# Kernel tuning notes

Measured on AMD Instinct MI355X. Metric: run time of the kernel, lower is better.

The kernel has to match this reference:

```python
import jax, jax.numpy as jnp
import numpy as np

DIM = 1024
B, L = 8, 2048
ACT = DIM // 4          # sparse_ratio 0.25
HID = DIM // 4          # LowRankFF reduction 4
EPS = 1e-6
K, DILATION = 5, 1
PAD = (K - 1) * DILATION // 2


def setup_inputs() -> dict:
    key = jax.random.key(0)
    ks = jax.random.split(key, 16)
    s = lambda fan_in: 1.0 / np.sqrt(fan_in)
    return {
        "x": jax.random.normal(ks[0], (B, L, DIM), jnp.float32),
        "norm_w": jnp.ones((DIM,), jnp.float32),
        "dw_w": jax.random.normal(ks[1], (DIM, 1, K), jnp.float32) * s(K),
        "dw_b": jax.random.normal(ks[2], (DIM,), jnp.float32) * s(K),
        "pw_w": jax.random.normal(ks[3], (DIM, DIM), jnp.float32) * s(DIM),
        "pw_b": jax.random.normal(ks[4], (DIM,), jnp.float32) * s(DIM),
        "alpha": jnp.full((ACT,), 0.9, jnp.float32),
        "beta": jnp.full((ACT,), 0.1, jnp.float32),
        "W1_w": jax.random.normal(ks[5], (DIM, DIM), jnp.float32) * s(DIM),
        "W1_b": jax.random.normal(ks[6], (DIM,), jnp.float32) * s(DIM),
        "W2_w": jax.random.normal(ks[7], (DIM, DIM), jnp.float32) * s(DIM),
        "W2_b": jax.random.normal(ks[8], (DIM,), jnp.float32) * s(DIM),
        "down_w": jax.random.normal(ks[9], (HID, DIM), jnp.float32) * s(DIM),
        "down_b": jax.random.normal(ks[10], (HID,), jnp.float32) * s(DIM),
        "up_w": jax.random.normal(ks[11], (DIM, HID), jnp.float32) * s(HID),
        "up_b": jax.random.normal(ks[12], (DIM,), jnpp := jnp.float32) * s(HID),
    }


def reference(x, norm_w, dw_w, dw_b, pw_w, pw_b, alpha, beta,
              W1_w, W1_b, W2_w, W2_b, down_w, down_b, up_w, up_b):
    residual = x
    # RMSNorm
    rms = jnp.sqrt(jnp.mean(x * x, axis=-1, keepdims=True) + EPS)
    xn = norm_w * (x / rms)                              # [B,L,D]
    # depthwise conv (groups=DIM), NCH layout; same-length output
    xc = jax.lax.conv_general_dilated(
        xn.transpose(0, 2, 1), dw_w,
        window_strides=(1,), padding=[(PAD, PAD)],
        rhs_dilation=(DILATION,), feature_group_count=DIM,
        dimension_numbers=("NCH", "OIH", "NCH")) + dw_b[None, :, None]
    xc = xc.transpose(0, 2, 1)                           # [B,L,D]
    # pointwise conv == dense linear over channels
    x_conv = jnp.einsum("bld,od->blo", xc, pw_w) + pw_b
    # sparse shift-gate recurrence on FIRST ACT channels (faithful to source)
    x_act = xn[:, :, :ACT]                               # [B,L,A]

    def step(h, xt):                                     # h,xt: [B,A]
        h = alpha * h + beta * xt
        return h, h

    _, hs = jax.lax.scan(step, jnp.zeros((B, ACT), xn.dtype),
                         x_act.transpose(1, 0, 2))       # hs: [L,B,A]
    x_rec = jnp.concatenate([hs.transpose(1, 0, 2), xn[:, :, ACT:]], axis=-1)
    # gated fusion
    y = x_conv + x_rec
    y = y + jax.nn.sigmoid(y @ W1_w.T + W1_b) * jnp.tanh(y @ W2_w.T + W2_b)
    # low-rank FF (exact gelu, matching torch F.gelu default)
    y = y + (jax.nn.gelu(y @ down_w.T + down_b, approximate=False) @ up_w.T + up_b)
    return y + residual
```

## Files before the change

kernel.cpp:

```cpp
#include <hip/hip_runtime.h>
#include <math.h>

#define DIMC 1024
#define BB   8
#define LL   2048
#define ACTC 256
#define HIDC 256
#define EPSV 1e-6f
#define MROWS (BB * LL)
#define NCHUNK 32
#define LC     64

typedef __bf16 bf16x8 __attribute__((ext_vector_type(8)));
typedef float  f32x4  __attribute__((ext_vector_type(4)));

__device__ __forceinline__ unsigned short f2bf(float f) {
    union { float f; unsigned int u; } v; v.f = f;
    unsigned int u = v.u + 0x7fffu + ((v.u >> 16) & 1u);
    return (unsigned short)(u >> 16);
}
__device__ __forceinline__ float bf2f(unsigned short s) {
    union { float f; unsigned int u; } v; v.u = ((unsigned int)s) << 16;
    return v.f;
}
__device__ __forceinline__ float fast_sigmoid(float x) {
    return 1.0f / (1.0f + __expf(-x));
}
__device__ __forceinline__ float fast_tanh(float x) {
    float ax = fabsf(x);
    float t = 1.0f - 2.0f / (__expf(2.0f * ax) + 1.0f);
    return copysignf(t, x);
}

__global__ void k_convert5(const float* __restrict__ s0, const float* __restrict__ s1,
                           const float* __restrict__ s2, const float* __restrict__ s3,
                           const float* __restrict__ s4,
                           unsigned short* __restrict__ d0, unsigned short* __restrict__ d1,
                           unsigned short* __restrict__ d2, unsigned short* __restrict__ d3,
                           unsigned short* __restrict__ d4) {
    int i = blockIdx.x * blockDim.x + threadIdx.x;
    if (i < 1048576)            d0[i]           = f2bf(s0[i]);
    else if (i < 2097152)       d1[i - 1048576] = f2bf(s1[i - 1048576]);
    else if (i < 3145728)       d2[i - 2097152] = f2bf(s2[i - 2097152]);
    else if (i < 3407872)       d3[i - 3145728] = f2bf(s3[i - 3145728]);
    else if (i < 3670016)       d4[i - 3407872] = f2bf(s4[i - 3407872]);
}

__global__ __launch_bounds__(256) void k_rmsnorm(const float* __restrict__ x,
                                                 const float* __restrict__ w,
                                                 unsigned short* __restrict__ xnb) {
    int m = blockIdx.x;
    int t = threadIdx.x;
    float4 v = ((const float4*)(x + (size_t)m * DIMC))[t];
    float ss = v.x*v.x + v.y*v.y + v.z*v.z + v.w*v.w;
#pragma unroll
    for (int off = 32; off > 0; off >>= 1) ss += __shfl_down(ss, off, 64);
    __shared__ float sred[4];
    if ((t & 63) == 0) sred[t >> 6] = ss;
    __syncthreads();
    float tot = sred[0] + sred[1] + sred[2] + sred[3];
    float rinv = 1.0f / sqrtf(tot * (1.0f / DIMC) + EPSV);
    float4 wv = ((const float4*)w)[t];
    uint2 o;
    o.x = (unsigned)f2bf(wv.x * v.x * rinv) | ((unsigned)f2bf(wv.y * v.y * rinv) << 16);
    o.y = (unsigned)f2bf(wv.z * v.z * rinv) | ((unsigned)f2bf(wv.w * v.w * rinv) << 16);
    ((uint2*)(xnb + (size_t)m * DIMC))[t] = o;
}

__global__ __launch_bounds__(256) void k_dwconv(const unsigned short* __restrict__ xnb,
                                                const float* __restrict__ dww,
                                                const float* __restrict__ dwb,
                                                unsigned short* __restrict__ xc) {
    int m = blockIdx.x;
    int l = m & (LL - 1);
    int t = threadIdx.x;
    int c0 = t * 4;
    float wgt[4][5];
#pragma unroll
    for (int j = 0; j < 4; ++j)
#pragma unroll
        for (int k = 0; k < 5; ++k) wgt[j][k] = dww[(c0 + j) * 5 + k];
    float4 bv = ((const float4*)dwb)[t];
    float acc[4] = {bv.x, bv.y, bv.z, bv.w};
#pragma unroll
    for (int k = 0; k < 5; ++k) {
        int ll = l + k - 2;
        if (ll < 0 || ll >= LL) continue;
        uint2 rv = ((const uint2*)(xnb + (size_t)(m + k - 2) * DIMC))[t];
        acc[0] += bf2f((unsigned short)(rv.x & 0xffff)) * wgt[0][k];
        acc[1] += bf2f((unsigned short)(rv.x >> 16))    * wgt[1][k];
        acc[2] += bf2f((unsigned short)(rv.y & 0xffff)) * wgt[2][k];
        acc[3] += bf2f((unsigned short)(rv.y >> 16))    * wgt[3][k];
    }
    uint2 o;
    o.x = (unsigned)f2bf(acc[0]) | ((unsigned)f2bf(acc[1]) << 16);
    o.y = (unsigned)f2bf(acc[2]) | ((unsigned)f2bf(acc[3]) << 16);
    ((uint2*)(xc + (size_t)m * DIMC))[t] = o;
}

__global__ __launch_bounds__(256) void k_scan_a(const unsigned short* __restrict__ xnb,
                                                const float* __restrict__ alpha,
                                                const float* __restrict__ beta,
                                                float* __restrict__ F) {
    int blk = blockIdx.x;
    int b = blk >> 5, k = blk & (NCHUNK - 1);
    int c = threadIdx.x;
    float a = alpha[c], bt = beta[c];
    const unsigned short* p = xnb + ((size_t)(b * LL + k * LC)) * DIMC + c;
    float h = 0.0f;
    for (int l = 0; l < LC; ++l) h = a * h + bt * bf2f(p[(size_t)l * DIMC]);
    F[(size_t)blk * ACTC + c] = h;
}
__global__ __launch_bounds__(256) void k_scan_b(const float* __restrict__ alpha,
                                                const float* __restrict__ F,
                                                float* __restrict__ Cv) {
    int b = blockIdx.x;
    int c = threadIdx.x;
    float a = alpha[c];
    float aL = a;
#pragma unroll
    for (int i = 0; i < 6; ++i) aL *= aL;
    float T = 0.0f;
    for (int k = 0; k < NCHUNK; ++k) {
        size_t idx = ((size_t)b * NCHUNK + k) * ACTC + c;
        Cv[idx] = T;
        T = F[idx] + aL * T;
    }
}
__global__ __launch_bounds__(256) void k_scan_c(const unsigned short* __restrict__ xnb,
                                                const float* __restrict__ alpha,
                                                const float* __restrict__ beta,
                                                const float* __restrict__ Cv,
                                                unsigned short* __restrict__ hs) {
    int blk = blockIdx.x;
    int b = blk >> 5, k = blk & (NCHUNK - 1);
    int c = threadIdx.x;
    float a = alpha[c], bt = beta[c];
    const unsigned short* p = xnb + ((size_t)(b * LL + k * LC)) * DIMC + c;
    unsigned short*       q = hs  + ((size_t)(b * LL + k * LC)) * ACTC + c;
    float h = Cv[(size_t)blk * ACTC + c];
    for (int l = 0; l < LC; ++l) {
        h = a * h + bt * bf2f(p[(size_t)l * DIMC]);
        q[(size_t)l * ACTC] = f2bf(h);
    }
}

#define TM 128
#define TN 128
#define BK 64

#define GLOAD_LDS(gp, lp) \
    __builtin_amdgcn_global_load_lds((const __attribute__((address_space(1))) unsigned int*)(gp), \
                                     (__attribute__((address_space(3))) unsigned int*)(lp), 16, 0, 0)

template<int MODE>
__global__ __launch_bounds__(256, (MODE == 1) ? 2 : 4) void k_gemm(
        const unsigned short* __restrict__ A,
        const unsigned short* __restrict__ B0,
        const unsigned short* __restrict__ B1,
        const float* __restrict__ bias0,
        const float* __restrict__ bias1,
        const unsigned short* __restrict__ add0,
        const unsigned short* __restrict__ add1,
        const float* __restrict__ addf,
        float* __restrict__ outf,
        unsigned short* __restrict__ outb,
        int M, int N, int K)
{
    constexpr int LDSB = (MODE == 1) ? 49152 : 32768;
    __shared__ __align__(16) char lds[LDSB];
    unsigned short* sA  = (unsigned short*)lds;
    unsigned short* sB0 = (unsigned short*)(lds + 16384);
    unsigned short* sB1 = (unsigned short*)(lds + 32768);

    int nx = gridDim.x;
    int bid = blockIdx.y * nx + blockIdx.x;
    int xcd = bid & 7, s = bid >> 3;
    int colt = s % nx, rowgrp = s / nx;
    int m0 = (rowgrp * 8 + xcd) * TM;
    int n0 = colt * TN;

    int t = threadIdx.x;
    int w = t >> 6, lane = t & 63;
    int wm = (w >> 1) * 64, wn = (w & 1) * 64;
    int quad = lane >> 4, lm = lane & 15;
    int lm7 = lm & 7;

    f32x4 zero = {0.f, 0.f, 0.f, 0.f};
    f32x4 acc0[4][4];
    f32x4 acc1[(MODE == 1) ? 4 : 1][(MODE == 1) ? 4 : 1];
#pragma unroll
    for (int i = 0; i < 4; ++i)
#pragma unroll
        for (int j = 0; j < 4; ++j) acc0[i][j] = zero;
    if constexpr (MODE == 1) {
#pragma unroll
        for (int i = 0; i < 4; ++i)
#pragma unroll
            for (int j = 0; j < 4; ++j) acc1[i][j] = zero;
    }

    for (int k0 = 0; k0 < K; k0 += BK) {
        __syncthreads();
#pragma unroll
        for (int c = 0; c < 4; ++c) {
            int i = t + c * 256;
            int r = i >> 3;
            int sc = ((i & 7) ^ (r & 7)) << 3;
            GLOAD_LDS(A  + (size_t)(m0 + r) * K + k0 + sc, sA  + i * 8);
            GLOAD_LDS(B0 + (size_t)(n0 + r) * K + k0 + sc, sB0 + i * 8);
            if constexpr (MODE == 1)
                GLOAD_LDS(B1 + (size_t)(n0 + r) * K + k0 + sc, sB1 + i * 8);
        }
        __syncthreads();

#pragma unroll
        for (int ks = 0; ks < BK; ks += 32) {
            int cgb = ks >> 3;
            bf16x8 af[4], b0f[4];
#pragma unroll
            for (int i = 0; i < 4; ++i) {
                int sg = ((cgb + quad) ^ lm7) << 3;
                af[i]  = *(const bf16x8*)(sA  + (wm + i * 16 + lm) * BK + sg);
                b0f[i] = *(const bf16x8*)(sB0 + (wn + i * 16 + lm) * BK + sg);
            }
            if constexpr (MODE == 1) {
                bf16x8 b1f[4];
#pragma unroll
                for (int i = 0; i < 4; ++i)
                    b1f[i] = *(const bf16x8*)(sB1 + (wn + i * 16 + lm) * BK + (((cgb + quad) ^ lm7) << 3));
#pragma unroll
                for (int mi = 0; mi < 4; ++mi)
#pragma unroll
                    for (int ni = 0; ni < 4; ++ni) {
                        acc0[mi][ni] = __builtin_amdgcn_mfma_f32_16x16x32_bf16(af[mi], b0f[ni], acc0[mi][ni], 0, 0, 0);
                        acc1[mi][ni] = __builtin_amdgcn_mfma_f32_16x16x32_bf16(af[mi], b1f[ni], acc1[mi][ni], 0, 0, 0);
                    }
            } else {
#pragma unroll
                for (int mi = 0; mi < 4; ++mi)
#pragma unroll
                    for (int ni = 0; ni < 4; ++ni)
                        acc0[mi][ni] = __builtin_amdgcn_mfma_f32_16x16x32_bf16(af[mi], b0f[ni], acc0[mi][ni], 0, 0, 0);
            }
        }
    }

    __syncthreads();
    if constexpr (MODE == 3) {
        float* sO = (float*)lds;
#pragma unroll
        for (int half = 0; half < 2; ++half) {
            if (wm == half * 64) {
#pragma unroll
                for (int mi = 0; mi < 4; ++mi) {
#pragma unroll
                    for (int ni = 0; ni < 4; ++ni) {
                        int nl = wn + ni * 16 + lm;
                        float bn = bias0[n0 + nl];
#pragma unroll
                        for (int j = 0; j < 4; ++j) {
                            int mloc = mi * 16 + quad * 4 + j;
                            sO[mloc * TN + nl] = acc0[mi][ni][j] + bn;
                        }
                    }
                }
            }
            __syncthreads();
#pragma unroll
            for (int c = 0; c < 8; ++c) {
                int i = t + c * 256;
                int r = i >> 5, c4 = (i & 31) << 2;
                int m = m0 + half * 64 + r, n = n0 + c4;
                float4 v  = *(float4*)(sO + r * TN + c4);
                uint2  ab = *(const uint2*)(add0 + (size_t)m * N + n);
                float4 xf = *(const float4*)(addf + (size_t)m * N + n);
                float4 o;
                o.x = v.x + bf2f((unsigned short)(ab.x & 0xffff)) + xf.x;
                o.y = v.y + bf2f((unsigned short)(ab.x >> 16))    + xf.y;
                o.z = v.z + bf2f((unsigned short)(ab.y & 0xffff)) + xf.z;
                o.w = v.w + bf2f((unsigned short)(ab.y >> 16))    + xf.w;
                *(float4*)(outf + (size_t)m * N + n) = o;
            }
            __syncthreads();
        }
    } else {
        unsigned short* sO = (unsigned short*)lds;
#pragma unroll
        for (int mi = 0; mi < 4; ++mi) {
#pragma unroll
            for (int ni = 0; ni < 4; ++ni) {
                int nl = wn + ni * 16 + lm;
                int n  = n0 + nl;
                float bn = bias0[n];
                float bn1 = (MODE == 1) ? bias1[n] : 0.0f;
#pragma unroll
                for (int j = 0; j < 4; ++j) {
                    int ml = wm + mi * 16 + quad * 4 + j;
                    float v = acc0[mi][ni][j];
                    float r;
                    if constexpr (MODE == 0) {
                        r = v + bn;
                    } else if constexpr (MODE == 1) {
                        float u1 = v + bn;
                        float u2 = acc1[mi][ni][j] + bn1;
                        r = fast_sigmoid(u1) * fast_tanh(u2);
                    } else {
                        float u = v + bn;
                        r = 0.5f * u * (1.0f + erff(u * 0.70710678118654752f));
                    }
                    sO[ml * TN + nl] = f2bf(r);
                }
            }
        }
        __syncthreads();
#pragma unroll
        for (int c = 0; c < 8; ++c) {
            int i = t + c * 256;
            int r = i >> 4, c8 = (i & 15) << 3;
            int m = m0 + r, n = n0 + c8;
            uint4 g = *(uint4*)(sO + r * TN + c8);
            if constexpr (MODE == 2) {
                *(uint4*)(outb + (size_t)m * N + n) = g;
            } else {
                uint4 av;
                if constexpr (MODE == 0) {
                    av = (n0 < ACTC) ? *(const uint4*)(add0 + (size_t)m * ACTC + n)
                                     : *(const uint4*)(add1 + (size_t)m * DIMC + n);
                } else {
                    av = *(const uint4*)(add0 + (size_t)m * N + n);
                }
                unsigned* gp = (unsigned*)&g;
                unsigned* ap = (unsigned*)&av;
                uint4 o;
                unsigned* op = (unsigned*)&o;
#pragma unroll
                for (int q = 0; q < 4; ++q) {
                    float lo = bf2f((unsigned short)(gp[q] & 0xffff)) + bf2f((unsigned short)(ap[q] & 0xffff));
                    float hi = bf2f((unsigned short)(gp[q] >> 16))    + bf2f((unsigned short)(ap[q] >> 16));
                    op[q] = (unsigned)f2bf(lo) | ((unsigned)f2bf(hi) << 16);
                }
                *(uint4*)(outb + (size_t)m * N + n) = o;
            }
        }
    }
}

extern "C" void kernel_launch(void* const* d_in, const int* in_sizes, int n_in,
                              void* d_out, int out_size, void* d_ws, size_t ws_size,
                              hipStream_t stream) {
    (void)in_sizes; (void)n_in; (void)out_size; (void)ws_size;
    const float* x      = (const float*)d_in[0];
    const float* norm_w = (const float*)d_in[1];
    const float* dw_w   = (const float*)d_in[2];
    const float* dw_b   = (const float*)d_in[3];
    const float* pw_w   = (const float*)d_in[4];
    const float* pw_b   = (const float*)d_in[5];
    const float* alpha  = (const float*)d_in[6];
    const float* beta   = (const float*)d_in[7];
    const float* W1_w   = (const float*)d_in[8];
    const float* W1_b   = (const float*)d_in[9];
    const float* W2_w   = (const float*)d_in[10];
    const float* W2_b   = (const float*)d_in[11];
    const float* down_w = (const float*)d_in[12];
    const float* down_b = (const float*)d_in[13];
    const float* up_w   = (const float*)d_in[14];
    const float* up_b   = (const float*)d_in[15];

    char* ws = (char*)d_ws;
    unsigned short* xnb  = (unsigned short*)(ws);
    unsigned short* xc   = (unsigned short*)(ws + 33554432ull);
    unsigned short* hs   = (unsigned short*)(ws + 67108864ull);
    unsigned short* y1b  = (unsigned short*)(ws + 75497472ull);
    unsigned short* y2b  = (unsigned short*)(ws + 109051904ull);
    unsigned short* gact = (unsigned short*)(ws + 142606336ull);
    unsigned short* wpw  = (unsigned short*)(ws + 150994944ull);
    unsigned short* w1b  = wpw + 1048576;
    unsigned short* w2b  = w1b + 1048576;
    unsigned short* wdn  = w2b + 1048576;
    unsigned short* wup  = wdn + 262144;
    float*          Fb   = (float*)(ws + 159383552ull);
    float*          Cb   = (float*)(ws + 159383552ull + 262144ull);

    k_convert5<<<14336, 256, 0, stream>>>(pw_w, W1_w, W2_w, down_w, up_w,
                                          wpw, w1b, w2b, wdn, wup);

    k_rmsnorm<<<MROWS, 256, 0, stream>>>(x, norm_w, xnb);
    k_dwconv <<<MROWS, 256, 0, stream>>>(xnb, dw_w, dw_b, xc);

    k_scan_a<<<BB * NCHUNK, ACTC, 0, stream>>>(xnb, alpha, beta, Fb);
    k_scan_b<<<BB, ACTC, 0, stream>>>(alpha, Fb, Cb);
    k_scan_c<<<BB * NCHUNK, ACTC, 0, stream>>>(xnb, alpha, beta, Cb, hs);

    dim3 g1(DIMC / TN, MROWS / TM);
    dim3 g2(HIDC / TN, MROWS / TM);
    k_gemm<0><<<g1, 256, 0, stream>>>(xc, wpw, nullptr, pw_b, nullptr, hs, xnb, nullptr, nullptr, y1b, MROWS, DIMC, DIMC);
    k_gemm<1><<<g1, 256, 0, stream>>>(y1b, w1b, w2b, W1_b, W2_b, y1b, nullptr, nullptr, nullptr, y2b, MROWS, DIMC, DIMC);
    k_gemm<2><<<g2, 256, 0, stream>>>(y2b, wdn, nullptr, down_b, nullptr, nullptr, nullptr, nullptr, nullptr, gact, MROWS, HIDC, DIMC);
    k_gemm<3><<<g1, 256, 0, stream>>>(gact, wup, nullptr, up_b, nullptr, y2b, nullptr, x, (float*)d_out, nullptr, MROWS, DIMC, HIDC);
}
```

Baseline: 375.5 us.

## Replace pointwise and gated GEMMs with 256-row tiled direct-to-LDS pipelined kernel

```diff
diff --git a/kernel.cpp b/kernel.cpp
--- a/kernel.cpp
+++ b/kernel.cpp
@@ -343,6 +343,206 @@
                 *(uint4*)(outb + (size_t)m * N + n) = o;
             }
         }
+    }
+}
+
+
+#define STG8(gb, rb, kq, dsto) \
+    __builtin_amdgcn_global_load_lds( \
+        (const __attribute__((address_space(1))) unsigned int*)((gb) + (size_t)(rb) * DIMC + (kq)), \
+        (__attribute__((address_space(3))) unsigned int*)(sb + (dsto) + (rb) * 64 + t * 8), 16, 0, 0)
+
+#define FENCE asm volatile("" ::: "memory")
+#define BAR   do { FENCE; __builtin_amdgcn_s_barrier(); FENCE; } while (0)
+
+#define READ_A(h, s) \
+    do { \
+        _Pragma("unroll") \
+        for (int i = 0; i < 4; ++i) { \
+            int ar = wm * 128 + (h) * 64 + i * 16 + lm; \
+            af[i] = *(const bf16x8*)(sb + bO + ar * 64 + ((((s) * 4 + quad) ^ lm7) << 3)); \
+        } \
+    } while (0)
+
+#define PHASE_MFMA(h, s) \
+    do { \
+        __builtin_amdgcn_s_setprio(1); \
+        _Pragma("unroll") \
+        for (int i = 0; i < 4; ++i) { \
+            _Pragma("unroll") \
+            for (int j = 0; j < NBF; ++j) { \
+                acc0[(h) * 4 + i][j] = __builtin_amdgcn_mfma_f32_16x16x32_bf16(af[i], bf0[s][j], acc0[(h) * 4 + i][j], 0, 0, 0); \
+                if constexpr (MODE == 1) \
+                    acc1[(h) * 4 + i][j] = __builtin_amdgcn_mfma_f32_16x16x32_bf16(af[i], bf1[s][j], acc1[(h) * 4 + i][j], 0, 0, 0); \
+            } \
+        } \
+        __builtin_amdgcn_s_setprio(0); \
+    } while (0)
+
+template<int MODE>
+__global__ __launch_bounds__(512, 1) void k_gemm8(
+        const unsigned short* __restrict__ A,
+        const unsigned short* __restrict__ B0,
+        const unsigned short* __restrict__ B1,
+        const float* __restrict__ bias0,
+        const float* __restrict__ bias1,
+        const unsigned short* __restrict__ add0,
+        const unsigned short* __restrict__ add1,
+        unsigned short* __restrict__ outb)
+{
+    constexpr int BN  = (MODE == 1) ? 128 : 256;
+    constexpr int WBN = BN / 4;
+    constexpr int NBF = WBN / 16;
+    constexpr int NTN = DIMC / BN;
+    constexpr int NT  = DIMC / 64;
+
+    extern __shared__ __align__(16) char lds[];
+    unsigned short* sb = (unsigned short*)lds;
+
+    int bid = blockIdx.x;
+    int xcd = bid & 7, sgrp = bid >> 3;
+    int colt = sgrp % NTN, rowgrp = sgrp / NTN;
+    int m0 = (rowgrp * 8 + xcd) * 256;
+    int n0 = colt * BN;
+
+    int t = threadIdx.x;
+    int w = t >> 6, lane = t & 63;
+    int wm = w >> 2, wn = w & 3;
+    int quad = lane >> 4, lm = lane & 15, lm7 = lm & 7;
+    int rl = t >> 3;
+    int scv = ((t & 7) ^ (rl & 7)) << 3;
+
+    const unsigned short* Ab  = A  + (size_t)(m0 + rl) * DIMC + scv;
+    const unsigned short* B0b = B0 + (size_t)(n0 + rl) * DIMC + scv;
+    const unsigned short* B1b = (MODE == 1) ? (B1 + (size_t)(n0 + rl) * DIMC + scv) : (const unsigned short*)0;
+
+    f32x4 zero = {0.f, 0.f, 0.f, 0.f};
+    f32x4 acc0[8][NBF];
+    f32x4 acc1[8][NBF];
+#pragma unroll
+    for (int i = 0; i < 8; ++i)
+#pragma unroll
+        for (int j = 0; j < NBF; ++j) acc0[i][j] = zero;
+    if constexpr (MODE == 1) {
+#pragma unroll
+        for (int i = 0; i < 8; ++i)
+#pragma unroll
+            for (int j = 0; j < NBF; ++j) acc1[i][j] = zero;
+    }
+
+    STG8(Ab, 0, 0, 0); STG8(Ab, 128, 0, 0);
+    STG8(B0b, 0, 0, 16384); STG8(B0b, 64, 0, 16384);
+    if constexpr (MODE == 0) { STG8(B0b, 128, 0, 16384); STG8(B0b, 192, 0, 16384); }
+    else                     { STG8(B1b, 0, 0, 24576);   STG8(B1b, 64, 0, 24576); }
+    STG8(Ab, 64, 0, 0); STG8(Ab, 192, 0, 0);
+    STG8(B0b, 0, 64, 32768 + 16384); STG8(B0b, 64, 64, 32768 + 16384);
+    STG8(Ab, 0, 64, 32768); STG8(Ab, 128, 64, 32768);
+    if constexpr (MODE == 0) { STG8(B0b, 128, 64, 32768 + 16384); STG8(B0b, 192, 64, 32768 + 16384); }
+    else                     { STG8(B1b, 0, 64, 32768 + 24576);   STG8(B1b, 64, 64, 32768 + 24576); }
+    asm volatile("s_waitcnt vmcnt(6)" ::: "memory");
+    BAR;
+
+    bf16x8 bf0[2][NBF];
+    bf16x8 bf1[2][NBF];
+
+#pragma unroll 2
+    for (int tau = 0; tau < NT; ++tau) {
+        const int bO  = (tau & 1) << 15;
+        const int bN  = ((tau & 1) ^ 1) << 15;
+        const int kq1 = (tau + 1) << 6;
+        const int kq2 = (tau + 2) << 6;
+        const bool g1v = (tau + 1 < NT), g2v = (tau + 2 < NT);
+        bf16x8 af[4];
+
+#pragma unroll
+        for (int ss = 0; ss < 2; ++ss)
+#pragma unroll
+            for (int j = 0; j < NBF; ++j) {
+                int br = wn * WBN + j * 16 + lm;
+                int sl = ((ss * 4 + quad) ^ lm7) << 3;
+                bf0[ss][j] = *(const bf16x8*)(sb + bO + 16384 + br * 64 + sl);
+                if constexpr (MODE == 1)
+                    bf1[ss][j] = *(const bf16x8*)(sb + bO + 24576 + br * 64 + sl);
+            }
+        READ_A(0, 0);
+        if (g1v) { STG8(Ab, 64, kq1, bN); STG8(Ab, 192, kq1, bN); }
+        BAR;
+        PHASE_MFMA(0, 0);
+        BAR;
+
+        READ_A(0, 1);
+        if (g2v) { STG8(B0b, 0, kq2, bO + 16384); STG8(B0b, 64, kq2, bO + 16384); }
+        BAR;
+        PHASE_MFMA(0, 1);
+        BAR;
+
+        READ_A(1, 0);
+        if (g2v) { STG8(Ab, 0, kq2, bO); STG8(Ab, 128, kq2, bO); }
+        BAR;
+        PHASE_MFMA(1, 0);
+        BAR;
+
+        READ_A(1, 1);
+        if (g2v) {
+            if constexpr (MODE == 0) { STG8(B0b, 128, kq2, bO + 16384); STG8(B0b, 192, kq2, bO + 16384); }
+            else                     { STG8(B1b, 0, kq2, bO + 24576);   STG8(B1b, 64, kq2, bO + 24576); }
+        }
+        BAR;
+        PHASE_MFMA(1, 1);
+        if (tau < NT - 2)        asm volatile("s_waitcnt vmcnt(6)" ::: "memory");
+        else if (tau == NT - 2)  asm volatile("s_waitcnt vmcnt(0)" ::: "memory");
+        BAR;
+    }
+
+    unsigned short* sO = sb;
+    __syncthreads();
+#pragma unroll
+    for (int mi = 0; mi < 8; ++mi) {
+#pragma unroll
+        for (int ni = 0; ni < NBF; ++ni) {
+            int nl = wn * WBN + ni * 16 + lm;
+            float bn = bias0[n0 + nl];
+            float bn1 = 0.f;
+            if constexpr (MODE == 1) bn1 = bias1[n0 + nl];
+#pragma unroll
+            for (int j = 0; j < 4; ++j) {
+                int ml = wm * 128 + mi * 16 + quad * 4 + j;
+                float r;
+                if constexpr (MODE == 0) {
+                    r = acc0[mi][ni][j] + bn;
+                } else {
+                    float u1 = acc0[mi][ni][j] + bn;
+                    float u2 = acc1[mi][ni][j] + bn1;
+                    r = fast_sigmoid(u1) * fast_tanh(u2);
+                }
+                sO[ml * BN + nl] = f2bf(r);
+            }
+        }
+    }
+    __syncthreads();
+#pragma unroll
+    for (int c = 0; c < ((MODE == 0) ? 16 : 8); ++c) {
+        int i = t + c * 512;
+        int r = i / (BN / 8);
+        int g = i % (BN / 8);
+        int m = m0 + r, n = n0 + g * 8;
+        uint4 gv = *(uint4*)(sO + r * BN + g * 8);
+        const unsigned short* ap;
+        if constexpr (MODE == 0)
+            ap = (colt == 0) ? (add0 + (size_t)m * ACTC + n) : (add1 + (size_t)m * DIMC + n);
+        else
+            ap = add0 + (size_t)m * DIMC + n;
+        uint4 av = *(const uint4*)ap;
+        unsigned* gp  = (unsigned*)&gv;
+        unsigned* app = (unsigned*)&av;
+        uint4 o; unsigned* op = (unsigned*)&o;
+#pragma unroll
+        for (int q = 0; q < 4; ++q) {
+            float lo = bf2f((unsigned short)(gp[q] & 0xffff)) + bf2f((unsigned short)(app[q] & 0xffff));
+            float hi = bf2f((unsigned short)(gp[q] >> 16))    + bf2f((unsigned short)(app[q] >> 16));
+            op[q] = (unsigned)f2bf(lo) | ((unsigned)f2bf(hi) << 16);
+        }
+        *(uint4*)(outb + (size_t)m * DIMC + n) = o;
     }
 }
 
@@ -382,6 +582,13 @@
     float*          Fb   = (float*)(ws + 159383552ull);
     float*          Cb   = (float*)(ws + 159383552ull + 262144ull);
 
+    static int attr_done = 0;
+    if (!attr_done) {
+        (void)hipFuncSetAttribute((const void*)&k_gemm8<0>, hipFuncAttributeMaxDynamicSharedMemorySize, 131072);
+        (void)hipFuncSetAttribute((const void*)&k_gemm8<1>, hipFuncAttributeMaxDynamicSharedMemorySize, 131072);
+        attr_done = 1;
+    }
+
     k_convert5<<<14336, 256, 0, stream>>>(pw_w, W1_w, W2_w, down_w, up_w,
                                           wpw, w1b, w2b, wdn, wup);
 
@@ -392,10 +599,13 @@
     k_scan_b<<<BB, ACTC, 0, stream>>>(alpha, Fb, Cb);
     k_scan_c<<<BB * NCHUNK, ACTC, 0, stream>>>(xnb, alpha, beta, Cb, hs);
 
+    k_gemm8<0><<<dim3((MROWS / 256) * (DIMC / 256)), dim3(512), 131072, stream>>>(
+        xc, wpw, nullptr, pw_b, nullptr, hs, xnb, y1b);
+    k_gemm8<1><<<dim3((MROWS / 256) * (DIMC / 128)), dim3(512), 131072, stream>>>(
+        y1b, w1b, w2b, W1_b, W2_b, y1b, nullptr, y2b);
+
     dim3 g1(DIMC / TN, MROWS / TM);
     dim3 g2(HIDC / TN, MROWS / TM);
-    k_gemm<0><<<g1, 256, 0, stream>>>(xc, wpw, nullptr, pw_b, nullptr, hs, xnb, nullptr, nullptr, y1b, MROWS, DIMC, DIMC);
-    k_gemm<1><<<g1, 256, 0, stream>>>(y1b, w1b, w2b, W1_b, W2_b, y1b, nullptr, nullptr, nullptr, y2b, MROWS, DIMC, DIMC);
     k_gemm<2><<<g2, 256, 0, stream>>>(y2b, wdn, nullptr, down_b, nullptr, nullptr, nullptr, nullptr, nullptr, gact, MROWS, HIDC, DIMC);
     k_gemm<3><<<g1, 256, 0, stream>>>(gact, wup, nullptr, up_b, nullptr, y2b, nullptr, x, (float*)d_out, nullptr, MROWS, DIMC, HIDC);
 }
```

After: 397.5 us. +5.8%, slower.

## Add narrow 64-column GEMM variant for gated and down-projection stages

Applied to the files above, without the earlier changes.

```diff
diff --git a/kernel.cpp b/kernel.cpp
--- a/kernel.cpp
+++ b/kernel.cpp
@@ -342,6 +342,155 @@
                 }
                 *(uint4*)(outb + (size_t)m * N + n) = o;
             }
+        }
+    }
+}
+
+template<int MODE>
+__global__ __launch_bounds__(256, (MODE == 1) ? 3 : 4) void k_gemm64(
+        const unsigned short* __restrict__ A,
+        const unsigned short* __restrict__ B0,
+        const unsigned short* __restrict__ B1,
+        const float* __restrict__ bias0,
+        const float* __restrict__ bias1,
+        const unsigned short* __restrict__ add0,
+        unsigned short* __restrict__ outb,
+        int M, int N, int K)
+{
+    constexpr int LDSB = (MODE == 1) ? 32768 : 24576;
+    __shared__ __align__(16) char lds[LDSB];
+    unsigned short* sA  = (unsigned short*)lds;
+    unsigned short* sB0 = (unsigned short*)(lds + 16384);
+    unsigned short* sB1 = (unsigned short*)(lds + 24576);
+
+    int nx = gridDim.x;
+    int bid = blockIdx.y * nx + blockIdx.x;
+    int xcd = bid & 7, s = bid >> 3;
+    int colt = s % nx, rowgrp = s / nx;
+    int m0 = (rowgrp * 8 + xcd) * TM;
+    int n0 = colt * 64;
+
+    int t = threadIdx.x;
+    int w = t >> 6, lane = t & 63;
+    int wm = (w >> 1) * 64, wn = (w & 1) * 32;
+    int quad = lane >> 4, lm = lane & 15;
+    int lm7 = lm & 7;
+
+    f32x4 zero = {0.f, 0.f, 0.f, 0.f};
+    f32x4 acc0[4][2];
+    f32x4 acc1[(MODE == 1) ? 4 : 1][(MODE == 1) ? 2 : 1];
+#pragma unroll
+    for (int i = 0; i < 4; ++i)
+#pragma unroll
+        for (int j = 0; j < 2; ++j) acc0[i][j] = zero;
+    if constexpr (MODE == 1) {
+#pragma unroll
+        for (int i = 0; i < 4; ++i)
+#pragma unroll
+            for (int j = 0; j < 2; ++j) acc1[i][j] = zero;
+    }
+
+    for (int k0 = 0; k0 < K; k0 += BK) {
+        __syncthreads();
+#pragma unroll
+        for (int c = 0; c < 4; ++c) {
+            int i = t + c * 256;
+            int r = i >> 3;
+            int sc = ((i & 7) ^ (r & 7)) << 3;
+            GLOAD_LDS(A + (size_t)(m0 + r) * K + k0 + sc, sA + i * 8);
+        }
+#pragma unroll
+        for (int c = 0; c < 2; ++c) {
+            int i = t + c * 256;
+            int r = i >> 3;
+            int sc = ((i & 7) ^ (r & 7)) << 3;
+            GLOAD_LDS(B0 + (size_t)(n0 + r) * K + k0 + sc, sB0 + i * 8);
+            if constexpr (MODE == 1)
+                GLOAD_LDS(B1 + (size_t)(n0 + r) * K + k0 + sc, sB1 + i * 8);
+        }
+        __syncthreads();
+
+#pragma unroll
+        for (int ks = 0; ks < BK; ks += 32) {
+            int cgb = ks >> 3;
+            int sg = ((cgb + quad) ^ lm7) << 3;
+            bf16x8 af[4], b0f[2];
+#pragma unroll
+            for (int i = 0; i < 4; ++i)
+                af[i] = *(const bf16x8*)(sA + (wm + i * 16 + lm) * BK + sg);
+#pragma unroll
+            for (int i = 0; i < 2; ++i)
+                b0f[i] = *(const bf16x8*)(sB0 + (wn + i * 16 + lm) * BK + sg);
+            if constexpr (MODE == 1) {
+                bf16x8 b1f[2];
+#pragma unroll
+                for (int i = 0; i < 2; ++i)
+                    b1f[i] = *(const bf16x8*)(sB1 + (wn + i * 16 + lm) * BK + sg);
+#pragma unroll
+                for (int mi = 0; mi < 4; ++mi)
+#pragma unroll
+                    for (int ni = 0; ni < 2; ++ni) {
+                        acc0[mi][ni] = __builtin_amdgcn_mfma_f32_16x16x32_bf16(af[mi], b0f[ni], acc0[mi][ni], 0, 0, 0);
+                        acc1[mi][ni] = __builtin_amdgcn_mfma_f32_16x16x32_bf16(af[mi], b1f[ni], acc1[mi][ni], 0, 0, 0);
+                    }
+            } else {
+#pragma unroll
+                for (int mi = 0; mi < 4; ++mi)
+#pragma unroll
+                    for (int ni = 0; ni < 2; ++ni)
+                        acc0[mi][ni] = __builtin_amdgcn_mfma_f32_16x16x32_bf16(af[mi], b0f[ni], acc0[mi][ni], 0, 0, 0);
+            }
+        }
+    }
+
+    __syncthreads();
+    unsigned short* sO = (unsigned short*)lds;
+#pragma unroll
+    for (int mi = 0; mi < 4; ++mi) {
+#pragma unroll
+        for (int ni = 0; ni < 2; ++ni) {
+            int nl = wn + ni * 16 + lm;
+            int n  = n0 + nl;
+            float bn = bias0[n];
+            float bn1 = (MODE == 1) ? bias1[n] : 0.0f;
+#pragma unroll
+            for (int j = 0; j < 4; ++j) {
+                int ml = wm + mi * 16 + quad * 4 + j;
+                float r;
+                if constexpr (MODE == 1) {
+                    float u1 = acc0[mi][ni][j] + bn;
+                    float u2 = acc1[mi][ni][j] + bn1;
+                    r = fast_sigmoid(u1) * fast_tanh(u2);
+                } else {
+                    float u = acc0[mi][ni][j] + bn;
+                    r = 0.5f * u * (1.0f + erff(u * 0.70710678118654752f));
+                }
+                sO[ml * 64 + nl] = f2bf(r);
+            }
+        }
+    }
+    __syncthreads();
+#pragma unroll
+    for (int c = 0; c < 4; ++c) {
+        int i = t + c * 256;
+        int r = i >> 3, c8 = (i & 7) << 3;
+        int m = m0 + r, n = n0 + c8;
+        uint4 g = *(uint4*)(sO + r * 64 + c8);
+        if constexpr (MODE == 2) {
+            *(uint4*)(outb + (size_t)m * N + n) = g;
+        } else {
+            uint4 av = *(const uint4*)(add0 + (size_t)m * N + n);
+            unsigned* gp = (unsigned*)&g;
+            unsigned* ap = (unsigned*)&av;
+            uint4 o;
+            unsigned* op = (unsigned*)&o;
+#pragma unroll
+            for (int q = 0; q < 4; ++q) {
+                float lo = bf2f((unsigned short)(gp[q] & 0xffff)) + bf2f((unsigned short)(ap[q] & 0xffff));
+                float hi = bf2f((unsigned short)(gp[q] >> 16))    + bf2f((unsigned short)(ap[q] >> 16));
+                op[q] = (unsigned)f2bf(lo) | ((unsigned)f2bf(hi) << 16);
+            }
+            *(uint4*)(outb + (size_t)m * N + n) = o;
         }
     }
 }
@@ -393,9 +542,10 @@
     k_scan_c<<<BB * NCHUNK, ACTC, 0, stream>>>(xnb, alpha, beta, Cb, hs);
 
     dim3 g1(DIMC / TN, MROWS / TM);
-    dim3 g2(HIDC / TN, MROWS / TM);
+    dim3 g1b(DIMC / 64, MROWS / TM);
+    dim3 g2b(HIDC / 64, MROWS / TM);
     k_gemm<0><<<g1, 256, 0, stream>>>(xc, wpw, nullptr, pw_b, nullptr, hs, xnb, nullptr, nullptr, y1b, MROWS, DIMC, DIMC);
-    k_gemm<1><<<g1, 256, 0, stream>>>(y1b, w1b, w2b, W1_b, W2_b, y1b, nullptr, nullptr, nullptr, y2b, MROWS, DIMC, DIMC);
-    k_gemm<2><<<g2, 256, 0, stream>>>(y2b, wdn, nullptr, down_b, nullptr, nullptr, nullptr, nullptr, nullptr, gact, MROWS, HIDC, DIMC);
+    k_gemm64<1><<<g1b, 256, 0, stream>>>(y1b, w1b, w2b, W1_b, W2_b, y1b, y2b, MROWS, DIMC, DIMC);
+    k_gemm64<2><<<g2b, 256, 0, stream>>>(y2b, wdn, nullptr, down_b, nullptr, nullptr, gact, MROWS, HIDC, DIMC);
     k_gemm<3><<<g1, 256, 0, stream>>>(gact, wup, nullptr, up_b, nullptr, y2b, nullptr, x, (float*)d_out, nullptr, MROWS, DIMC, HIDC);
 }
```

Measured after the change: 379.8 us. No clear change (+1.1%).
